# Kernel optimization log

Hardware: AMD Instinct MI355X
Metric: run time of the kernel (lower is better)

Reference implementation:

```python
import jax, jax.numpy as jnp
import numpy as np

NHEAD = 8
TOP_K = 2


def layernorm(x, g, b, eps=1e-5):
    m = x.mean(-1, keepdims=True)
    v = x.var(-1, keepdims=True)
    return (x - m) * jax.lax.rsqrt(v + eps) * g + b


def causal_conv(x, w, b, dil):
    # x: [N, C, L], w: [O, I, K] (torch layout), left-pad for causality
    pad = (w.shape[-1] - 1) * dil
    y = jax.lax.conv_general_dilated(x, w, (1,), [(pad, 0)], rhs_dilation=(dil,),
                                     dimension_numbers=('NCH', 'OIH', 'NCH'))
    return y + b[None, :, None]


def sinusoidal_pe(L, d):
    pos = jnp.arange(L, dtype=jnp.float32)[:, None]
    div = jnp.exp(jnp.arange(0, d, 2, dtype=jnp.float32) * (-np.log(10000.0) / d))
    pe = jnp.zeros((L, d), jnp.float32)
    pe = pe.at[:, 0::2].set(jnp.sin(pos * div))
    pe = pe.at[:, 1::2].set(jnp.cos(pos * div))
    return pe


def _forward(x, sensor_mask, enc_proj_w, enc_proj_b, tcn_w1, tcn_b1, tcn_w2, tcn_b2,
             enc_norm_g, enc_norm_b, pool_proj_w, pool_proj_b, pos_inter,
             t_wq, t_bq, t_wk, t_bk, t_wv, t_bv, t_wo, t_bo,
             t_ln1_g, t_ln1_b, t_ln2_g, t_ln2_b,
             t_ff1_w, t_ff1_b, t_ff2_w, t_ff2_b, t_out_g, t_out_b,
             exp_w1, exp_b1, exp_w2, exp_b2,
             gate_f_w, gate_f_b, gate_fail_w, gate_fail_b, gate_rca_w, gate_rca_b,
             pred_w, pred_b, fail_w, fail_b, rca_w, rca_b):
    B, L, M = x.shape
    P = enc_proj_w.shape[1]
    D = pool_proj_w.shape[1]
    O = exp_w2.shape[-1]
    # mask sensors, grab last value per sensor (globally standardized)
    xm = jnp.transpose(x, (0, 2, 1)) * sensor_mask[:, :, None]        # [B, M, L]
    last_val = xm[:, :, -1]                                           # [B, M]
    seqs = xm.reshape(B * M, L, 1)
    # per-sensor TCN encoder
    h = seqs @ enc_proj_w + enc_proj_b                                # [BM, L, P]
    h = h + sinusoidal_pe(L, P)[None]
    h = jnp.transpose(h, (0, 2, 1))                                   # [BM, P, L]
    for i in range(tcn_w1.shape[0]):
        dil = 2 ** i
        out = jax.nn.relu(causal_conv(h, tcn_w1[i], tcn_b1[i], dil))
        out = jax.nn.relu(causal_conv(out, tcn_w2[i], tcn_b2[i], dil))
        h = jax.nn.relu(out + h)                                      # channels equal -> identity residual
    h = layernorm(jnp.transpose(h, (0, 2, 1)), enc_norm_g, enc_norm_b)  # [BM, L, T]
    feats = h.reshape(B, M, L, -1) * sensor_mask[:, :, None, None]
    pooled = feats.mean(axis=2)                                       # [B, M, T]
    t = pooled @ pool_proj_w + pool_proj_b                            # [B, M, D]
    # inter-sensor transformer (pre-LN), key padding mask where sensor_mask==0
    t = t + pos_inter[:, :M, :]
    bias = jnp.where(sensor_mask == 0, -1e9, 0.0)[:, None, None, :]   # [B,1,1,M]
    dh = D // NHEAD
    for l in range(t_wq.shape[0]):
        y = layernorm(t, t_ln1_g[l], t_ln1_b[l])
        q = (y @ t_wq[l] + t_bq[l]).reshape(B, M, NHEAD, dh)
        k = (y @ t_wk[l] + t_bk[l]).reshape(B, M, NHEAD, dh)
        v = (y @ t_wv[l] + t_bv[l]).reshape(B, M, NHEAD, dh)
        s = jnp.einsum('bqhd,bkhd->bhqk', q, k) / jnp.sqrt(jnp.float32(dh)) + bias
        a = jax.nn.softmax(s, axis=-1)
        o = jnp.einsum('bhqk,bkhd->bqhd', a, v).reshape(B, M, D) @ t_wo[l] + t_bo[l]
        t = t + o
        y2 = layernorm(t, t_ln2_g[l], t_ln2_b[l])
        t = t + jax.nn.relu(y2 @ t_ff1_w[l] + t_ff1_b[l]) @ t_ff2_w[l] + t_ff2_b[l]
    ctx = layernorm(t, t_out_g, t_out_b) * sensor_mask[:, :, None]    # [B, M, D]
    # global context: masked mean + masked max over valid sensors
    cnt = jnp.maximum(sensor_mask.sum(1, keepdims=True), 1.0)
    mean_ctx = ctx.sum(1) / cnt                                       # [B, D]
    max_ctx = jnp.where(sensor_mask[:, :, None] > 0, ctx, -1e9).max(1)
    g = jnp.concatenate([mean_ctx, max_ctx], -1)                      # [B, 2D]

    def moe(x_exp, gate_in, gw, gb):
        logits = gate_in @ gw + gb                                    # [N, E]
        vals, idx = jax.lax.top_k(logits, TOP_K)
        w = jax.nn.softmax(vals, -1)
        hh = jax.nn.relu(jnp.einsum('nd,edh->neh', x_exp, exp_w1) + exp_b1)
        allo = jnp.einsum('neh,eho->neo', hh, exp_w2) + exp_b2        # [N, E, O]
        sel = jnp.take_along_axis(allo, idx[..., None], axis=1)
        return (sel * w[..., None]).sum(1)                            # [N, O]

    y_f = moe(g, g, gate_f_w, gate_f_b)                               # [B, O]
    y_fail = moe(g, g, gate_fail_w, gate_fail_b)
    tok = ctx.reshape(B * M, D)
    exp_in_rca = jnp.concatenate(
        [tok, jnp.broadcast_to(mean_ctx[:, None, :], (B, M, D)).reshape(B * M, D)], -1)
    y_rca = moe(exp_in_rca, tok, gate_rca_w, gate_rca_b).reshape(B, M, O)
    # heads
    pred_in = jnp.concatenate([pooled, ctx, jnp.broadcast_to(y_f[:, None, :], (B, M, O))], -1)
    pred = pred_in @ pred_w + pred_b + last_val[..., None]            # [B, M, PH]
    fail_out = y_fail @ fail_w + fail_b                               # [B, FH]
    rca_in = jnp.concatenate([pooled, ctx, y_rca], -1)
    rca_out = (rca_in @ rca_w + rca_b)[..., 0]                        # [B, M]
    return jnp.concatenate([pred.reshape(B, -1), fail_out, rca_out], axis=1)


def setup_inputs() -> dict:
    key = jax.random.key(0)
    ks = iter(jax.random.split(key, 64))
    nrm = lambda shape, s=0.05: jax.random.normal(next(ks), shape, jnp.float32) * s
    B, L, M = 16, 512, 32
    P, T, D, E, EH, O = 64, 64, 128, 16, 512, 128
    NL, LEV, K = 2, 4, 3
    return dict(
        x=jax.random.normal(next(ks), (B, L, M), jnp.float32),
        sensor_mask=jax.random.randint(next(ks), (B, M), 0, 2).astype(jnp.float32),
        enc_proj_w=nrm((1, P)), enc_proj_b=jnp.zeros((P,)),
        tcn_w1=nrm((LEV, P, P, K)), tcn_b1=jnp.zeros((LEV, P)),
        tcn_w2=nrm((LEV, P, P, K)), tcn_b2=jnp.zeros((LEV, P)),
        enc_norm_g=jnp.ones((T,)), enc_norm_b=jnp.zeros((T,)),
        pool_proj_w=nrm((T, D)), pool_proj_b=jnp.zeros((D,)),
        pos_inter=nrm((1, M, D), 0.02),
        t_wq=nrm((NL, D, D)), t_bq=jnp.zeros((NL, D)),
        t_wk=nrm((NL, D, D)), t_bk=jnp.zeros((NL, D)),
        t_wv=nrm((NL, D, D)), t_bv=jnp.zeros((NL, D)),
        t_wo=nrm((NL, D, D)), t_bo=jnp.zeros((NL, D)),
        t_ln1_g=jnp.ones((NL, D)), t_ln1_b=jnp.zeros((NL, D)),
        t_ln2_g=jnp.ones((NL, D)), t_ln2_b=jnp.zeros((NL, D)),
        t_ff1_w=nrm((NL, D, 2 * D)), t_ff1_b=jnp.zeros((NL, 2 * D)),
        t_ff2_w=nrm((NL, 2 * D, D)), t_ff2_b=jnp.zeros((NL, D)),
        t_out_g=jnp.ones((D,)), t_out_b=jnp.zeros((D,)),
        exp_w1=nrm((E, 2 * D, EH)), exp_b1=jnp.zeros((E, EH)),
        exp_w2=nrm((E, EH, O)), exp_b2=jnp.zeros((E, O)),
        gate_f_w=nrm((2 * D, E)), gate_f_b=jnp.zeros((E,)),
        gate_fail_w=nrm((2 * D, E)), gate_fail_b=jnp.zeros((E,)),
        gate_rca_w=nrm((D, E)), gate_rca_b=jnp.zeros((E,)),
        pred_w=nrm((T + D + O, 3)), pred_b=jnp.zeros((3,)),
        fail_w=nrm((O, 3)), fail_b=jnp.zeros((3,)),
        rca_w=nrm((T + D + O, 1)), rca_b=jnp.zeros((1,)),
    )


def reference(x, sensor_mask, enc_proj_w, enc_proj_b, tcn_w1, tcn_b1, tcn_w2, tcn_b2,
              enc_norm_g, enc_norm_b, pool_proj_w, pool_proj_b, pos_inter,
              t_wq, t_bq, t_wk, t_bk, t_wv, t_bv, t_wo, t_bo,
              t_ln1_g, t_ln1_b, t_ln2_g, t_ln2_b,
              t_ff1_w, t_ff1_b, t_ff2_w, t_ff2_b, t_out_g, t_out_b,
              exp_w1, exp_b1, exp_w2, exp_b2,
              gate_f_w, gate_f_b, gate_fail_w, gate_fail_b, gate_rca_w, gate_rca_b,
              pred_w, pred_b, fail_w, fail_b, rca_w, rca_b):
    return _forward(x, sensor_mask, enc_proj_w, enc_proj_b, tcn_w1, tcn_b1, tcn_w2, tcn_b2,
                    enc_norm_g, enc_norm_b, pool_proj_w, pool_proj_b, pos_inter,
                    t_wq, t_bq, t_wk, t_bk, t_wv, t_bv, t_wo, t_bo,
                    t_ln1_g, t_ln1_b, t_ln2_g, t_ln2_b,
                    t_ff1_w, t_ff1_b, t_ff2_w, t_ff2_b, t_out_g, t_out_b,
                    exp_w1, exp_b1, exp_w2, exp_b2,
                    gate_f_w, gate_f_b, gate_fail_w, gate_fail_b, gate_rca_w, gate_rca_b,
                    pred_w, pred_b, fail_w, fail_b, rca_w, rca_b)
```

## Files before the change

kernel.cpp:

```cpp
#include <hip/hip_runtime.h>
#include <hip/hip_bf16.h>

#define B_   16
#define L_   512
#define M_   32
#define P_   64
#define D_   128
#define NH_  8
#define NL_  2
#define E_   16
#define EH_  512
#define O_   128

#define PADF  16
#define ROWSF 528
#define LDW   64

typedef short  bf16x8 __attribute__((ext_vector_type(8)));
typedef float  f32x4  __attribute__((ext_vector_type(4)));
typedef unsigned short us4 __attribute__((ext_vector_type(4)));
typedef unsigned short us8 __attribute__((ext_vector_type(8)));

__device__ __forceinline__ float bf2f(unsigned short h) {
  unsigned u = ((unsigned)h) << 16; float f; __builtin_memcpy(&f, &u, 4); return f;
}
__device__ __forceinline__ unsigned short f2bf(float f) {
  unsigned u; __builtin_memcpy(&u, &f, 4);
  u += 0x7fffu + ((u >> 16) & 1);
  return (unsigned short)(u >> 16);
}
__device__ __forceinline__ int swz(int row, int col_us) {
  return row * LDW + (col_us ^ ((row & 7) << 3));
}

#define XFW_PPW   0
#define XFW_QKVO  8192
#define XFW_F1    139264
#define XFW_F2    204800

__global__ __launch_bounds__(256) void prep_kernel(
    const float* __restrict__ ppw,
    const float* __restrict__ twq, const float* __restrict__ twk,
    const float* __restrict__ twv, const float* __restrict__ two,
    const float* __restrict__ f1w, const float* __restrict__ f2w,
    const float* __restrict__ ew1, const float* __restrict__ ew2,
    const float* __restrict__ tw1, const float* __restrict__ tw2,
    unsigned short* __restrict__ xfw, unsigned short* __restrict__ w1t,
    unsigned short* __restrict__ w2t, unsigned short* __restrict__ wpack,
    float* __restrict__ peT) {
  const int b = blockIdx.x;
  const int tid = threadIdx.x;
  if (b < 834) {
    __shared__ float tl[64][65];
    const float* src; unsigned short* dst; int R, C, tr, tc;
    if (b < 2) {
      src = ppw; dst = xfw + XFW_PPW; R = 64; C = 128; tr = 0; tc = b;
    } else if (b < 34) {
      int t = b - 2; int lg = t >> 2; int l = lg >> 2, gem = lg & 3;
      int tt = t & 3; tr = tt >> 1; tc = tt & 1;
      const float* s4 = (gem == 0) ? twq : (gem == 1) ? twk : (gem == 2) ? twv : two;
      src = s4 + l * 16384; dst = xfw + XFW_QKVO + l * 65536 + gem * 16384; R = 128; C = 128;
    } else if (b < 50) {
      int t = b - 34; int l = t >> 3; int tt = t & 7; tr = tt >> 2; tc = tt & 3;
      src = f1w + l * 32768; dst = xfw + XFW_F1 + l * 32768; R = 128; C = 256;
    } else if (b < 66) {
      int t = b - 50; int l = t >> 3; int tt = t & 7; tr = tt >> 1; tc = tt & 1;
      src = f2w + l * 32768; dst = xfw + XFW_F2 + l * 32768; R = 256; C = 128;
    } else if (b < 578) {
      int t = b - 66; int e = t >> 5; int tt = t & 31; tr = tt >> 3; tc = tt & 7;
      src = ew1 + e * 131072; dst = w1t + e * 131072; R = 256; C = 512;
    } else {
      int t = b - 578; int e = t >> 4; int tt = t & 15; tr = tt >> 1; tc = tt & 1;
      src = ew2 + e * 65536; dst = w2t + e * 65536; R = 512; C = 128;
    }
    for (int i = tid; i < 4096; i += 256) {
      int r = i >> 6, c = i & 63;
      tl[r][c] = src[(tr * 64 + r) * C + tc * 64 + c];
    }
    __syncthreads();
    for (int i = tid; i < 4096; i += 256) {
      int c = i >> 6, r = i & 63;
      dst[(tc * 64 + c) * R + tr * 64 + r] = f2bf(tl[r][c]);
    }
  } else if (b < 840) {
    int base = (b - 834) * 16384;
    for (int q = tid; q < 16384; q += 256) {
      int i = base + q;
      int c = i & 63, o = (i >> 6) & 63, tlc = i >> 12;
      int t = tlc % 3, lc = tlc / 3, lvl = lc >> 1;
      const float* src = (lc & 1) ? tw2 : tw1;
      wpack[i] = f2bf(src[lvl * 12288 + o * 192 + c * 3 + t]);
    }
  } else {
    int base = (b - 840) * 16384;
    for (int q = tid; q < 16384; q += 256) {
      int j = base + q; int ll = j >> 6, c = j & 63;
      float dv = expf(-0.14391157f * (float)(c & ~1));
      float ang = (float)ll * dv;
      peT[j] = (c & 1) ? cosf(ang) : sinf(ang);
    }
  }
}

template <int DIL, bool RES>
__device__ __forceinline__ void conv_gw(const unsigned short* __restrict__ IN,
                                        unsigned short* __restrict__ OUT,
                                        const unsigned short* __restrict__ wp,
                                        const float* __restrict__ bias) {
  const int tid  = threadIdx.x;
  const int wid  = tid >> 6;
  const int lane = tid & 63;
  const int fr   = lane & 15;
  const int g    = lane >> 4;
  const int ot0  = (wid & 1) * 2;
  const int ng   = wid >> 1;

  bf16x8 Af[2][6];
#pragma unroll
  for (int oo = 0; oo < 2; ++oo)
#pragma unroll
    for (int t = 0; t < 3; ++t)
#pragma unroll
      for (int kh = 0; kh < 2; ++kh)
        Af[oo][t * 2 + kh] =
            *(const bf16x8*)(wp + (t * 64 + (ot0 + oo) * 16 + fr) * 64 + kh * 32 + g * 8);
  float bv[2][4];
#pragma unroll
  for (int oo = 0; oo < 2; ++oo)
#pragma unroll
    for (int j = 0; j < 4; ++j) bv[oo][j] = bias[(ot0 + oo) * 16 + g * 4 + j];

#pragma unroll
  for (int k = 0; k < 4; ++k) {
    const int rb = PADF + (ng + k * 8) * 16 + fr;
    bf16x8 Bf[6];
#pragma unroll
    for (int t = 0; t < 3; ++t) {
      int r = rb + (t - 2) * DIL;
#pragma unroll
      for (int kh = 0; kh < 2; ++kh)
        Bf[t * 2 + kh] = *(const bf16x8*)(IN + swz(r, kh * 32 + g * 8));
    }
    f32x4 acc[2];
#pragma unroll
    for (int oo = 0; oo < 2; ++oo) {
      f32x4 a; a[0] = bv[oo][0]; a[1] = bv[oo][1]; a[2] = bv[oo][2]; a[3] = bv[oo][3];
      acc[oo] = a;
    }
#pragma unroll
    for (int f = 0; f < 6; ++f)
#pragma unroll
      for (int oo = 0; oo < 2; ++oo)
        acc[oo] = __builtin_amdgcn_mfma_f32_16x16x32_bf16(Af[oo][f], Bf[f], acc[oo], 0, 0, 0);

#pragma unroll
    for (int oo = 0; oo < 2; ++oo) {
      unsigned short* op = OUT + swz(rb, (ot0 + oo) * 16 + g * 4);
      us4 old;
      if (RES) old = *(const us4*)op;
      us4 st;
#pragma unroll
      for (int j = 0; j < 4; ++j) {
        float v = fmaxf(acc[oo][j], 0.f);
        if (RES) v = fmaxf(v + bf2f(old[j]), 0.f);
        st[j] = f2bf(v);
      }
      *(us4*)op = st;
    }
  }
}

__global__ __launch_bounds__(1024) void tcn_kernel(
    const float* __restrict__ x, const float* __restrict__ mask,
    const float* __restrict__ pw, const float* __restrict__ pb,
    const unsigned short* __restrict__ wpack,
    const float* __restrict__ b1, const float* __restrict__ b2,
    const float* __restrict__ peT,
    const float* __restrict__ lng, const float* __restrict__ lnb,
    float* __restrict__ psum) {
  extern __shared__ unsigned short smu[];
  unsigned short* A  = smu;
  unsigned short* Bq = A + ROWSF * LDW;
  float* pwpb = (float*)(Bq + ROWSF * LDW);
  float* mst  = pwpb + 128;
  float* pp   = mst + 1024;

  const int seq = blockIdx.x;
  const int b = seq >> 5;
  const int m = seq & 31;
  if (mask[b * M_ + m] == 0.0f) return;
  const int tid = threadIdx.x;

  if (tid < 64)        pwpb[tid] = pw[tid];
  else if (tid < 128)  pwpb[tid] = pb[tid - 64];
  __syncthreads();

  if (tid < ROWSF) {
    int r = tid;
    if (r >= PADF) {
      int l = r - PADF;
      float xv = x[(b * L_ + l) * M_ + m];
      const float4* pe4 = (const float4*)(peT + l * 64);
#pragma unroll
      for (int c0 = 0; c0 < 64; c0 += 8) {
        float4 pa = pe4[c0 / 4], pc = pe4[c0 / 4 + 1];
        float pe[8] = {pa.x, pa.y, pa.z, pa.w, pc.x, pc.y, pc.z, pc.w};
        us8 st;
#pragma unroll
        for (int j = 0; j < 8; ++j) {
          int c = c0 + j;
          st[j] = f2bf(fmaf(xv, pwpb[c], pwpb[64 + c]) + pe[j]);
        }
        *(us8*)(A + swz(r, c0)) = st;
      }
    } else {
      us8 z = {0, 0, 0, 0, 0, 0, 0, 0};
#pragma unroll
      for (int c0 = 0; c0 < 64; c0 += 8) {
        *(us8*)(A + swz(r, c0)) = z;
        *(us8*)(Bq + swz(r, c0)) = z;
      }
    }
  }
  __syncthreads();

  conv_gw<1, false>(A, Bq, wpack + 0 * 12288, b1 + 0);   __syncthreads();
  conv_gw<1, true >(Bq, A, wpack + 1 * 12288, b2 + 0);   __syncthreads();
  conv_gw<2, false>(A, Bq, wpack + 2 * 12288, b1 + 64);  __syncthreads();
  conv_gw<2, true >(Bq, A, wpack + 3 * 12288, b2 + 64);  __syncthreads();
  conv_gw<4, false>(A, Bq, wpack + 4 * 12288, b1 + 128); __syncthreads();
  conv_gw<4, true >(Bq, A, wpack + 5 * 12288, b2 + 128); __syncthreads();
  conv_gw<8, false>(A, Bq, wpack + 6 * 12288, b1 + 192); __syncthreads();
  conv_gw<8, true >(Bq, A, wpack + 7 * 12288, b2 + 192); __syncthreads();

  if (tid < 512) {
    int r = PADF + tid;
    float s = 0.f, ss = 0.f;
#pragma unroll
    for (int c0 = 0; c0 < 64; c0 += 8) {
      bf16x8 vv = *(const bf16x8*)(A + swz(r, c0));
#pragma unroll
      for (int j = 0; j < 8; ++j) { float v = bf2f((unsigned short)vv[j]); s += v; ss += v * v; }
    }
    float mu = s * 0.015625f;
    float var = fmaxf(ss * 0.015625f - mu * mu, 0.0f);
    mst[tid] = mu;
    mst[512 + tid] = rsqrtf(var + 1e-5f);
  }
  __syncthreads();
  {
    int p = tid & 63, q = tid >> 6;
    float accp = 0.f;
    int r0 = PADF + q * 32;
    for (int r = r0; r < r0 + 32; ++r)
      accp += (bf2f(A[swz(r, p)]) - mst[r - PADF]) * mst[512 + r - PADF];
    pp[tid] = accp;
  }
  __syncthreads();
  if (tid < 64) {
    float acc = 0.f;
#pragma unroll
    for (int q = 0; q < 16; ++q) acc += pp[q * 64 + tid];
    psum[seq * 64 + tid] = lng[tid] * acc + 512.0f * lnb[tid];
  }
}

__global__ __launch_bounds__(1024) void xf_kernel(
    const float* __restrict__ psum, const float* __restrict__ mask,
    const unsigned short* __restrict__ xfw,
    const float* __restrict__ ppb, const float* __restrict__ pos,
    const float* __restrict__ bq, const float* __restrict__ bk,
    const float* __restrict__ bv, const float* __restrict__ bo,
    const float* __restrict__ l1g, const float* __restrict__ l1b,
    const float* __restrict__ l2g, const float* __restrict__ l2b,
    const float* __restrict__ f1b, const float* __restrict__ f2b,
    const float* __restrict__ og_, const float* __restrict__ ob_,
    const float* __restrict__ gfw, const float* __restrict__ gfb,
    const float* __restrict__ glw, const float* __restrict__ glb,
    const float* __restrict__ grw, const float* __restrict__ grb,
    float* __restrict__ pooledws, float* __restrict__ ctxws,
    float* __restrict__ gwt, int* __restrict__ ecnt, int* __restrict__ elist,
    unsigned short* __restrict__ xbf) {
  extern __shared__ float sm[];
  float* T    = sm;
  float* QKV  = T + 4224;
  float* S    = QKV + 12672;
  float* gv   = S + 8448;
  float* mkv  = gv + 512;
  unsigned short* Ybf = (unsigned short*)(mkv + 64);
  unsigned short* Yb2 = Ybf + 32 * 136;
  unsigned short* FFH = Yb2 + 32 * 136;
  const int b = blockIdx.x;
  const int tid = threadIdx.x;
  const int wid = tid >> 6;
  const int lane = tid & 63;
  const int fr = lane & 15;
  const int g = lane >> 4;
  const int row32 = tid >> 5;
  const int ln32  = tid & 31;

  if (tid < 32) mkv[tid] = mask[b * 32 + tid];
  for (int idx = tid; idx < 2048; idx += 1024) {
    int mm = idx >> 6, p = idx & 63;
    float v = psum[(b * 32 + mm) * 64 + p] * mask[b * 32 + mm] * (1.0f / 512.0f);
    pooledws[(b * 32 + mm) * 64 + p] = v;
    Ybf[mm * 136 + p] = f2bf(v);
  }
  __syncthreads();

  {
    int mt = wid >> 3, nt = wid & 7;
    bf16x8 Af[2];
#pragma unroll
    for (int kf = 0; kf < 2; ++kf)
      Af[kf] = *(const bf16x8*)(Ybf + (mt * 16 + fr) * 136 + kf * 32 + g * 8);
    const unsigned short* bp = xfw + XFW_PPW + (nt * 16 + fr) * 64;
    f32x4 acc = {0.f, 0.f, 0.f, 0.f};
#pragma unroll
    for (int kf = 0; kf < 2; ++kf)
      acc = __builtin_amdgcn_mfma_f32_16x16x32_bf16(Af[kf], *(const bf16x8*)(bp + kf * 32 + g * 8), acc, 0, 0, 0);
    int n = nt * 16 + fr;
    float bb = ppb[n];
#pragma unroll
    for (int j = 0; j < 4; ++j) {
      int m = mt * 16 + g * 4 + j;
      T[m * 132 + n] = acc[j] + bb + pos[m * 128 + n];
    }
  }
  __syncthreads();

#define LN_BF(GAMMA, BETA)                                                     \
  {                                                                            \
    int mm = row32, j0 = ln32 * 4;                                             \
    float4 v4 = *(const float4*)(T + mm * 132 + j0);                           \
    float s = v4.x + v4.y + v4.z + v4.w;                                       \
    float ss = v4.x * v4.x + v4.y * v4.y + v4.z * v4.z + v4.w * v4.w;          \
    _Pragma("unroll") for (int mk = 16; mk >= 1; mk >>= 1) {                   \
      s += __shfl_xor(s, mk); ss += __shfl_xor(ss, mk);                        \
    }                                                                          \
    float mu = s * 0.0078125f;                                                 \
    float rstd = rsqrtf(fmaxf(ss * 0.0078125f - mu * mu, 0.f) + 1e-5f);        \
    us4 st;                                                                    \
    float vv[4] = {v4.x, v4.y, v4.z, v4.w};                                    \
    _Pragma("unroll") for (int j = 0; j < 4; ++j)                              \
      st[j] = f2bf((vv[j] - mu) * rstd * (GAMMA)[j0 + j] + (BETA)[j0 + j]);    \
    *(us4*)(Ybf + mm * 136 + j0) = st;                                         \
  }                                                                            \
  __syncthreads();

  for (int l = 0; l < NL_; ++l) {
    LN_BF(l1g + l * 128, l1b + l * 128)
#pragma unroll
    for (int i = 0; i < 3; ++i) {
      int tt = wid * 3 + i;
      int gem = tt >> 4, r = tt & 15, mt = r >> 3, nt = r & 7;
      const unsigned short* wT = xfw + XFW_QKVO + l * 65536 + gem * 16384;
      const float* bias = (gem == 0) ? bq : (gem == 1) ? bk : bv;
      bf16x8 Afr[4];
#pragma unroll
      for (int kf = 0; kf < 4; ++kf)
        Afr[kf] = *(const bf16x8*)(Ybf + (mt * 16 + fr) * 136 + kf * 32 + g * 8);
      const unsigned short* bp = wT + (nt * 16 + fr) * 128;
      f32x4 acc = {0.f, 0.f, 0.f, 0.f};
#pragma unroll
      for (int kf = 0; kf < 4; ++kf)
        acc = __builtin_amdgcn_mfma_f32_16x16x32_bf16(Afr[kf], *(const bf16x8*)(bp + kf * 32 + g * 8), acc, 0, 0, 0);
      int n = nt * 16 + fr;
      float bb = bias[l * 128 + n];
#pragma unroll
      for (int j = 0; j < 4; ++j)
        QKV[(mt * 16 + g * 4 + j) * 396 + gem * 132 + n] = acc[j] + bb;
    }
    __syncthreads();

    {
      int n = ln32;
      float mbias = (mkv[n] == 0.0f) ? -1e9f : 0.f;
#pragma unroll
      for (int t = 0; t < 8; ++t) {
        int task = row32 * 8 + t;
        int h = task >> 5, mm = task & 31;
        const float* qp = QKV + mm * 396 + h * 16;
        const float* kp = QKV + n * 396 + 132 + h * 16;
        float a = 0;
#pragma unroll
        for (int d = 0; d < 16; ++d) a = fmaf(qp[d], kp[d], a);
        a = a * 0.25f + mbias;
        float mx = a;
#pragma unroll
        for (int mk = 16; mk >= 1; mk >>= 1) mx = fmaxf(mx, __shfl_xor(mx, mk));
        float e = __expf(a - mx);
        float sum = e;
#pragma unroll
        for (int mk = 16; mk >= 1; mk >>= 1) sum += __shfl_xor(sum, mk);
        S[h * 1056 + mm * 33 + n] = e / sum;
      }
    }
    __syncthreads();

    {
      int mm = row32, j0 = ln32 * 4, h = j0 >> 4;
      const float* sp = S + h * 1056 + mm * 33;
      f32x4 a = {0.f, 0.f, 0.f, 0.f};
#pragma unroll 8
      for (int n = 0; n < 32; ++n) {
        float p = sp[n];
        float4 v4 = *(const float4*)(QKV + n * 396 + 264 + j0);
        a[0] = fmaf(p, v4.x, a[0]); a[1] = fmaf(p, v4.y, a[1]);
        a[2] = fmaf(p, v4.z, a[2]); a[3] = fmaf(p, v4.w, a[3]);
      }
      us4 st;
#pragma unroll
      for (int j = 0; j < 4; ++j) st[j] = f2bf(a[j]);
      *(us4*)(Yb2 + mm * 136 + j0) = st;
    }
    __syncthreads();

    {
      int mt = wid >> 3, nt = wid & 7;
      bf16x8 Aw[4];
#pragma unroll
      for (int kf = 0; kf < 4; ++kf)
        Aw[kf] = *(const bf16x8*)(Yb2 + (mt * 16 + fr) * 136 + kf * 32 + g * 8);
      const unsigned short* bp = xfw + XFW_QKVO + l * 65536 + 3 * 16384 + (nt * 16 + fr) * 128;
      f32x4 acc = {0.f, 0.f, 0.f, 0.f};
#pragma unroll
      for (int kf = 0; kf < 4; ++kf)
        acc = __builtin_amdgcn_mfma_f32_16x16x32_bf16(Aw[kf], *(const bf16x8*)(bp + kf * 32 + g * 8), acc, 0, 0, 0);
      int n = nt * 16 + fr;
      float bb = bo[l * 128 + n];
#pragma unroll
      for (int j = 0; j < 4; ++j)
        T[(mt * 16 + g * 4 + j) * 132 + n] += acc[j] + bb;
    }
    __syncthreads();

    LN_BF(l2g + l * 128, l2b + l * 128)
#pragma unroll
    for (int i = 0; i < 2; ++i) {
      int tt = wid * 2 + i;
      int mt = tt >> 4, nt = tt & 15;
      bf16x8 Aff[4];
#pragma unroll
      for (int kf = 0; kf < 4; ++kf)
        Aff[kf] = *(const bf16x8*)(Ybf + (mt * 16 + fr) * 136 + kf * 32 + g * 8);
      const unsigned short* bp = xfw + XFW_F1 + l * 32768 + (nt * 16 + fr) * 128;
      f32x4 acc = {0.f, 0.f, 0.f, 0.f};
#pragma unroll
      for (int kf = 0; kf < 4; ++kf)
        acc = __builtin_amdgcn_mfma_f32_16x16x32_bf16(Aff[kf], *(const bf16x8*)(bp + kf * 32 + g * 8), acc, 0, 0, 0);
      int n = nt * 16 + fr;
      float bb = f1b[l * 256 + n];
#pragma unroll
      for (int j = 0; j < 4; ++j)
        FFH[(mt * 16 + g * 4 + j) * 264 + n] = f2bf(fmaxf(acc[j] + bb, 0.f));
    }
    __syncthreads();
    {
      int mt = wid >> 3, nt = wid & 7;
      bf16x8 Af2[8];
#pragma unroll
      for (int kf = 0; kf < 8; ++kf)
        Af2[kf] = *(const bf16x8*)(FFH + (mt * 16 + fr) * 264 + kf * 32 + g * 8);
      const unsigned short* bp = xfw + XFW_F2 + l * 32768 + (nt * 16 + fr) * 256;
      f32x4 acc = {0.f, 0.f, 0.f, 0.f};
#pragma unroll
      for (int kf = 0; kf < 8; ++kf)
        acc = __builtin_amdgcn_mfma_f32_16x16x32_bf16(Af2[kf], *(const bf16x8*)(bp + kf * 32 + g * 8), acc, 0, 0, 0);
      int n = nt * 16 + fr;
      float bb = f2b[l * 128 + n];
#pragma unroll
      for (int j = 0; j < 4; ++j)
        T[(mt * 16 + g * 4 + j) * 132 + n] += acc[j] + bb;
    }
    __syncthreads();
  }
#undef LN_BF

  {
    int mm = row32, j0 = ln32 * 4;
    float4 v4 = *(const float4*)(T + mm * 132 + j0);
    float s = v4.x + v4.y + v4.z + v4.w;
    float ss = v4.x * v4.x + v4.y * v4.y + v4.z * v4.z + v4.w * v4.w;
#pragma unroll
    for (int mk = 16; mk >= 1; mk >>= 1) { s += __shfl_xor(s, mk); ss += __shfl_xor(ss, mk); }
    float mu = s * 0.0078125f;
    float rstd = rsqrtf(fmaxf(ss * 0.0078125f - mu * mu, 0.f) + 1e-5f);
    float mk_ = mkv[mm];
    float vv[4] = {v4.x, v4.y, v4.z, v4.w};
#pragma unroll
    for (int j = 0; j < 4; ++j) {
      float c = ((vv[j] - mu) * rstd * og_[j0 + j] + ob_[j0 + j]) * mk_;
      S[mm * 132 + j0 + j] = c;
      ctxws[(b * 32 + mm) * 128 + j0 + j] = c;
    }
  }
  __syncthreads();
  if (tid < 128) {
    float cnt = 0;
    for (int mm = 0; mm < 32; ++mm) cnt += mkv[mm];
    cnt = fmaxf(cnt, 1.0f);
    float s = 0, mx = -1e9f;
    for (int mm = 0; mm < 32; ++mm) {
      float v = S[mm * 132 + tid];
      s += v;
      if (mkv[mm] > 0.0f) mx = fmaxf(mx, v);
    }
    gv[tid] = s / cnt;
    gv[128 + tid] = mx;
  }
  __syncthreads();

  float* lg = QKV;
  if (tid < 544) {
    int lr = tid >> 4, e = tid & 15;
    float a;
    if (lr == 0) {
      a = gfb[e];
      for (int d = 0; d < 256; ++d) a = fmaf(gv[d], gfw[d * 16 + e], a);
    } else if (lr == 1) {
      a = glb[e];
      for (int d = 0; d < 256; ++d) a = fmaf(gv[d], glw[d * 16 + e], a);
    } else {
      int mm = lr - 2;
      a = grb[e];
      for (int d = 0; d < 128; ++d) a = fmaf(S[mm * 132 + d], grw[d * 16 + e], a);
    }
    lg[lr * 16 + e] = a;
  }
  __syncthreads();
  if (tid < 34) {
    const float* lgr = lg + tid * 16;
    int i0 = 0; float v0 = lgr[0];
    for (int e = 1; e < 16; ++e) if (lgr[e] > v0) { v0 = lgr[e]; i0 = e; }
    int i1 = (i0 == 0) ? 1 : 0; float v1 = lgr[i1];
    for (int e = 0; e < 16; ++e) if (e != i0 && lgr[e] > v1) { v1 = lgr[e]; i1 = e; }
    float e1 = __expf(v1 - v0);
    float w0 = 1.0f / (1.0f + e1);
    int gr = (tid == 0) ? b : (tid == 1) ? (16 + b) : (32 + b * 32 + (tid - 2));
    gwt[2 * gr] = w0;  gwt[2 * gr + 1] = 1.0f - w0;
    int p0 = atomicAdd(&ecnt[i0], 1); elist[i0 * 544 + p0] = 2 * gr;
    int p1 = atomicAdd(&ecnt[i1], 1); elist[i1 * 544 + p1] = 2 * gr + 1;
  }
  for (int j = tid; j < 34 * 256; j += 1024) {
    int lr = j >> 8, d = j & 255;
    float v;
    if (lr < 2) v = gv[d];
    else        v = (d < 128) ? S[(lr - 2) * 132 + d] : gv[d - 128];
    int gr = (lr == 0) ? b : (lr == 1) ? (16 + b) : (32 + b * 32 + (lr - 2));
    xbf[gr * 256 + d] = f2bf(v);
  }
}

__global__ __launch_bounds__(512) void moe_kernel(
    const unsigned short* __restrict__ xbf, const float* __restrict__ gwt,
    const int* __restrict__ elist, const int* __restrict__ ecnt,
    const unsigned short* __restrict__ w1t, const float* __restrict__ eb1,
    const unsigned short* __restrict__ w2t, const float* __restrict__ eb2,
    float* __restrict__ yall) {
  __shared__ unsigned short Xb[16 * 264];
  __shared__ unsigned short Hb[16 * 520];
  __shared__ float wl[16];
  __shared__ int rowl[16];
  const int e = blockIdx.x >> 3;
  const int slot = blockIdx.x & 7;
  const int n = ecnt[e];
  const int ntiles = (n + 15) >> 4;
  const int tid = threadIdx.x;
  const int wid = tid >> 6;
  const int lane = tid & 63;
  const int fr = lane & 15;
  const int g = lane >> 4;

  for (int t = slot; t < ntiles; t += 8) {
    if (tid < 16) {
      int idx = t * 16 + tid;
      int id = (idx < n) ? elist[e * 544 + idx] : -1;
      rowl[tid] = (id >= 0) ? (id >> 1) : -1;
      wl[tid] = (id >= 0) ? gwt[id] : 0.f;
    }
    __syncthreads();
    for (int i = tid; i < 512; i += 512) {
      int r = i >> 5, c8 = (i & 31) * 8;
      int row = rowl[r];
      bf16x8 v = {0, 0, 0, 0, 0, 0, 0, 0};
      if (row >= 0) v = *(const bf16x8*)(xbf + row * 256 + c8);
      *(bf16x8*)(Xb + r * 264 + c8) = v;
    }
    __syncthreads();
    bf16x8 Af[8];
#pragma unroll
    for (int kf = 0; kf < 8; ++kf)
      Af[kf] = *(const bf16x8*)(Xb + fr * 264 + kf * 32 + g * 8);
#pragma unroll
    for (int ntl = 0; ntl < 4; ++ntl) {
      int nt = wid * 4 + ntl;
      const unsigned short* bp = w1t + (e * 512 + nt * 16 + fr) * 256;
      f32x4 acc = {0.f, 0.f, 0.f, 0.f};
#pragma unroll
      for (int kf = 0; kf < 8; ++kf)
        acc = __builtin_amdgcn_mfma_f32_16x16x32_bf16(Af[kf], *(const bf16x8*)(bp + kf * 32 + g * 8), acc, 0, 0, 0);
      int h = nt * 16 + fr;
      float b1v = eb1[e * 512 + h];
#pragma unroll
      for (int j = 0; j < 4; ++j)
        Hb[(g * 4 + j) * 520 + h] = f2bf(fmaxf(acc[j] + b1v, 0.f));
    }
    __syncthreads();
    {
      const unsigned short* bp = w2t + (e * 128 + wid * 16 + fr) * 512;
      f32x4 acc = {0.f, 0.f, 0.f, 0.f};
#pragma unroll
      for (int kf = 0; kf < 16; ++kf) {
        bf16x8 Ah = *(const bf16x8*)(Hb + fr * 520 + kf * 32 + g * 8);
        acc = __builtin_amdgcn_mfma_f32_16x16x32_bf16(Ah, *(const bf16x8*)(bp + kf * 32 + g * 8), acc, 0, 0, 0);
      }
      int o = wid * 16 + fr;
      float b2v = eb2[e * 128 + o];
#pragma unroll
      for (int j = 0; j < 4; ++j) {
        int r = g * 4 + j;
        int row = rowl[r];
        if (row >= 0) atomicAdd(&yall[row * 128 + o], wl[r] * (acc[j] + b2v));
      }
    }
    __syncthreads();
  }
}

__global__ __launch_bounds__(192) void heads_kernel(
    const float* __restrict__ x, const float* __restrict__ mask,
    const float* __restrict__ pooledws, const float* __restrict__ ctxws,
    const float* __restrict__ yf, const float* __restrict__ yfail, const float* __restrict__ yrca,
    const float* __restrict__ pw, const float* __restrict__ pb,
    const float* __restrict__ fw, const float* __restrict__ fb,
    const float* __restrict__ rw, const float* __restrict__ rb,
    float* __restrict__ out) {
  __shared__ float yfb[128];
  int b = blockIdx.x, t = threadIdx.x;
  if (t < 128) yfb[t] = yf[b * 128 + t];
  __syncthreads();
  if (t < 96) {
    int mm = t / 3, o = t - mm * 3;
    int s = b * 32 + mm;
    float a = pb[o];
    const float* pl = pooledws + s * 64;
    for (int i = 0; i < 64; ++i) a = fmaf(pl[i], pw[i * 3 + o], a);
    const float* cx = ctxws + s * 128;
    for (int i = 0; i < 128; ++i) a = fmaf(cx[i], pw[(64 + i) * 3 + o], a);
    for (int i = 0; i < 128; ++i) a = fmaf(yfb[i], pw[(192 + i) * 3 + o], a);
    a += x[(b * 512 + 511) * 32 + mm] * mask[b * 32 + mm];
    out[b * 131 + t] = a;
  } else if (t < 99) {
    int o = t - 96;
    float a = fb[o];
    const float* yl = yfail + b * 128;
    for (int i = 0; i < 128; ++i) a = fmaf(yl[i], fw[i * 3 + o], a);
    out[b * 131 + 96 + o] = a;
  } else if (t < 131) {
    int mm = t - 99;
    int s = b * 32 + mm;
    float a = rb[0];
    const float* pl = pooledws + s * 64;
    for (int i = 0; i < 64; ++i) a = fmaf(pl[i], rw[i], a);
    const float* cx = ctxws + s * 128;
    for (int i = 0; i < 128; ++i) a = fmaf(cx[i], rw[64 + i], a);
    const float* yr = yrca + s * 128;
    for (int i = 0; i < 128; ++i) a = fmaf(yr[i], rw[192 + i], a);
    out[b * 131 + 99 + mm] = a;
  }
}

extern "C" void kernel_launch(void* const* d_in, const int* in_sizes, int n_in,
                              void* d_out, int out_size, void* d_ws, size_t ws_size,
                              hipStream_t stream) {
  (void)in_sizes; (void)n_in; (void)out_size; (void)ws_size;
  const float* x    = (const float*)d_in[0];
  const float* msk  = (const float*)d_in[1];
  const float* epw  = (const float*)d_in[2];
  const float* epb  = (const float*)d_in[3];
  const float* tw1  = (const float*)d_in[4];
  const float* tb1  = (const float*)d_in[5];
  const float* tw2  = (const float*)d_in[6];
  const float* tb2  = (const float*)d_in[7];
  const float* eng  = (const float*)d_in[8];
  const float* enb  = (const float*)d_in[9];
  const float* ppw  = (const float*)d_in[10];
  const float* ppb  = (const float*)d_in[11];
  const float* pos  = (const float*)d_in[12];
  const float* twq  = (const float*)d_in[13];
  const float* tbq  = (const float*)d_in[14];
  const float* twk  = (const float*)d_in[15];
  const float* tbk  = (const float*)d_in[16];
  const float* twv  = (const float*)d_in[17];
  const float* tbv  = (const float*)d_in[18];
  const float* two  = (const float*)d_in[19];
  const float* tbo  = (const float*)d_in[20];
  const float* l1g  = (const float*)d_in[21];
  const float* l1b  = (const float*)d_in[22];
  const float* l2g  = (const float*)d_in[23];
  const float* l2b  = (const float*)d_in[24];
  const float* f1w  = (const float*)d_in[25];
  const float* f1b  = (const float*)d_in[26];
  const float* f2w  = (const float*)d_in[27];
  const float* f2b  = (const float*)d_in[28];
  const float* tog  = (const float*)d_in[29];
  const float* tob  = (const float*)d_in[30];
  const float* ew1  = (const float*)d_in[31];
  const float* eb1  = (const float*)d_in[32];
  const float* ew2  = (const float*)d_in[33];
  const float* eb2  = (const float*)d_in[34];
  const float* gfw  = (const float*)d_in[35];
  const float* gfb  = (const float*)d_in[36];
  const float* glw  = (const float*)d_in[37];
  const float* glb  = (const float*)d_in[38];
  const float* grw  = (const float*)d_in[39];
  const float* grb  = (const float*)d_in[40];
  const float* prw  = (const float*)d_in[41];
  const float* prb  = (const float*)d_in[42];
  const float* fw   = (const float*)d_in[43];
  const float* fb   = (const float*)d_in[44];
  const float* rw   = (const float*)d_in[45];
  const float* rb   = (const float*)d_in[46];

  float* ws      = (float*)d_ws;
  float* psum    = ws;
  float* pooledw = psum + 32768;
  float* ctxw    = pooledw + 32768;
  float* yall    = ctxw + 65536;
  float* gwt     = yall + 69632;
  int*   ecnt    = (int*)(gwt + 1088);
  int*   elist   = ecnt + 16;
  float* peT     = (float*)(elist + 8704);
  unsigned short* wpack = (unsigned short*)(peT + 32768);
  unsigned short* xfw   = wpack + 98304;
  unsigned short* w1t   = xfw + 270336;
  unsigned short* w2t   = w1t + 2097152;
  unsigned short* xbf   = w2t + 1048576;

  const int tcn_lds = 2 * ROWSF * LDW * 2 + (128 + 1024 + 1024) * 4;
  const int xf_lds  = (4224 + 12672 + 8448 + 512 + 64) * 4 + (2 * 4352 + 8448) * 2;
  hipFuncSetAttribute((const void*)tcn_kernel, hipFuncAttributeMaxDynamicSharedMemorySize, tcn_lds);
  hipFuncSetAttribute((const void*)xf_kernel,  hipFuncAttributeMaxDynamicSharedMemorySize, xf_lds);

  hipMemsetAsync(yall, 0, 69632 * sizeof(float), stream);
  hipMemsetAsync(ecnt, 0, 16 * sizeof(int), stream);

  prep_kernel<<<842, 256, 0, stream>>>(ppw, twq, twk, twv, two, f1w, f2w, ew1, ew2,
                                       tw1, tw2, xfw, w1t, w2t, wpack, peT);
  tcn_kernel<<<512, 1024, tcn_lds, stream>>>(x, msk, epw, epb, wpack, tb1, tb2, peT,
                                             eng, enb, psum);
  xf_kernel<<<16, 1024, xf_lds, stream>>>(psum, msk, xfw, ppb, pos,
                                          tbq, tbk, tbv, tbo,
                                          l1g, l1b, l2g, l2b, f1b, f2b,
                                          tog, tob,
                                          gfw, gfb, glw, glb, grw, grb,
                                          pooledw, ctxw, gwt, ecnt, elist, xbf);
  moe_kernel<<<128, 512, 0, stream>>>(xbf, gwt, elist, ecnt, w1t, eb1, w2t, eb2, yall);
  heads_kernel<<<16, 192, 0, stream>>>(x, msk, pooledw, ctxw,
                                       yall, yall + 2048, yall + 4096,
                                       prw, prb, fw, fb, rw, rb, (float*)d_out);
}
```

Before: 290.2 us.

## Stage TCN conv weights in LDS with register prefetch; fold memsets into prep

The TCN kernel now stages each level's packed conv weights into a swizzled LDS buffer. The next level's weights are prefetched from global memory into registers while the current convolution runs, replacing per-wave global loads of the A fragments. The LN scratch now aliases the weight buffer, which shrinks LDS, and waves_per_eu is set for occupancy. The two hipMemsetAsync calls are folded into extra prep_kernel blocks, and the workspace layout is shifted, at the cost of extra register pressure and syncs per phase.

```diff
diff --git a/kernel.cpp b/kernel.cpp
--- a/kernel.cpp
+++ b/kernel.cpp
@@ -47,7 +47,7 @@
     const float* __restrict__ tw1, const float* __restrict__ tw2,
     unsigned short* __restrict__ xfw, unsigned short* __restrict__ w1t,
     unsigned short* __restrict__ w2t, unsigned short* __restrict__ wpack,
-    float* __restrict__ peT) {
+    float* __restrict__ peT, float* __restrict__ yall, int* __restrict__ ecnt) {
   const int b = blockIdx.x;
   const int tid = threadIdx.x;
   if (b < 834) {
@@ -91,7 +91,7 @@
       const float* src = (lc & 1) ? tw2 : tw1;
       wpack[i] = f2bf(src[lvl * 12288 + o * 192 + c * 3 + t]);
     }
-  } else {
+  } else if (b < 842) {
     int base = (b - 840) * 16384;
     for (int q = tid; q < 16384; q += 256) {
       int j = base + q; int ll = j >> 6, c = j & 63;
@@ -99,14 +99,23 @@
       float ang = (float)ll * dv;
       peT[j] = (c & 1) ? cosf(ang) : sinf(ang);
     }
+  } else {
+    int j = b - 842;
+    if (j < 68) {
+      for (int q = tid; q < 1024; q += 256) yall[j * 1024 + q] = 0.f;
+    } else {
+      if (tid < 16) ecnt[tid] = 0;
+    }
   }
 }
 
 template <int DIL, bool RES>
-__device__ __forceinline__ void conv_gw(const unsigned short* __restrict__ IN,
-                                        unsigned short* __restrict__ OUT,
-                                        const unsigned short* __restrict__ wp,
-                                        const float* __restrict__ bias) {
+__device__ __forceinline__ void conv_phase(const unsigned short* __restrict__ IN,
+                                           unsigned short* __restrict__ OUT,
+                                           unsigned short* __restrict__ Wb,
+                                           const float* __restrict__ bias,
+                                           float4* wreg, bool do_store,
+                                           const unsigned short* __restrict__ wload) {
   const int tid  = threadIdx.x;
   const int wid  = tid >> 6;
   const int lane = tid & 63;
@@ -121,14 +130,28 @@
 #pragma unroll
     for (int t = 0; t < 3; ++t)
 #pragma unroll
-      for (int kh = 0; kh < 2; ++kh)
-        Af[oo][t * 2 + kh] =
-            *(const bf16x8*)(wp + (t * 64 + (ot0 + oo) * 16 + fr) * 64 + kh * 32 + g * 8);
+      for (int kh = 0; kh < 2; ++kh) {
+        int wr = t * 64 + (ot0 + oo) * 16 + fr;
+        Af[oo][t * 2 + kh] = *(const bf16x8*)(Wb + swz(wr, kh * 32 + g * 8));
+      }
   float bv[2][4];
 #pragma unroll
   for (int oo = 0; oo < 2; ++oo)
 #pragma unroll
     for (int j = 0; j < 4; ++j) bv[oo][j] = bias[(ot0 + oo) * 16 + g * 4 + j];
+
+  __syncthreads();
+
+  if (do_store) {
+    *(float4*)(Wb + swz(tid >> 3, (tid & 7) * 8)) = wreg[0];
+    if (tid < 512)
+      *(float4*)(Wb + swz((tid >> 3) + 128, (tid & 7) * 8)) = wreg[1];
+  }
+  if (wload) {
+    wreg[0] = *(const float4*)(wload + (tid >> 3) * 64 + (tid & 7) * 8);
+    if (tid < 512)
+      wreg[1] = *(const float4*)(wload + ((tid >> 3) + 128) * 64 + (tid & 7) * 8);
+  }
 
 #pragma unroll
   for (int k = 0; k < 4; ++k) {
@@ -168,9 +191,12 @@
       *(us4*)op = st;
     }
   }
-}
-
-__global__ __launch_bounds__(1024) void tcn_kernel(
+  __syncthreads();
+}
+
+__global__ __attribute__((amdgpu_flat_work_group_size(1024, 1024),
+                          amdgpu_waves_per_eu(4, 4)))
+void tcn_kernel(
     const float* __restrict__ x, const float* __restrict__ mask,
     const float* __restrict__ pw, const float* __restrict__ pb,
     const unsigned short* __restrict__ wpack,
@@ -181,8 +207,9 @@
   extern __shared__ unsigned short smu[];
   unsigned short* A  = smu;
   unsigned short* Bq = A + ROWSF * LDW;
-  float* pwpb = (float*)(Bq + ROWSF * LDW);
-  float* mst  = pwpb + 128;
+  unsigned short* Wb = Bq + ROWSF * LDW;
+  float* pwpb = (float*)(Wb + 192 * LDW);
+  float* mst  = (float*)Wb;
   float* pp   = mst + 1024;
 
   const int seq = blockIdx.x;
@@ -191,8 +218,12 @@
   if (mask[b * M_ + m] == 0.0f) return;
   const int tid = threadIdx.x;
 
-  if (tid < 64)        pwpb[tid] = pw[tid];
-  else if (tid < 128)  pwpb[tid] = pb[tid - 64];
+  float4 wreg[2];
+  wreg[0] = *(const float4*)(wpack + (tid >> 3) * 64 + (tid & 7) * 8);
+  if (tid < 512)
+    wreg[1] = *(const float4*)(wpack + ((tid >> 3) + 128) * 64 + (tid & 7) * 8);
+  if (tid < 64)       pwpb[tid] = pw[tid];
+  else if (tid < 128) pwpb[tid] = pb[tid - 64];
   __syncthreads();
 
   if (tid < ROWSF) {
@@ -224,14 +255,24 @@
   }
   __syncthreads();
 
-  conv_gw<1, false>(A, Bq, wpack + 0 * 12288, b1 + 0);   __syncthreads();
-  conv_gw<1, true >(Bq, A, wpack + 1 * 12288, b2 + 0);   __syncthreads();
-  conv_gw<2, false>(A, Bq, wpack + 2 * 12288, b1 + 64);  __syncthreads();
-  conv_gw<2, true >(Bq, A, wpack + 3 * 12288, b2 + 64);  __syncthreads();
-  conv_gw<4, false>(A, Bq, wpack + 4 * 12288, b1 + 128); __syncthreads();
-  conv_gw<4, true >(Bq, A, wpack + 5 * 12288, b2 + 128); __syncthreads();
-  conv_gw<8, false>(A, Bq, wpack + 6 * 12288, b1 + 192); __syncthreads();
-  conv_gw<8, true >(Bq, A, wpack + 7 * 12288, b2 + 192); __syncthreads();
+  {
+    *(float4*)(Wb + swz(tid >> 3, (tid & 7) * 8)) = wreg[0];
+    if (tid < 512)
+      *(float4*)(Wb + swz((tid >> 3) + 128, (tid & 7) * 8)) = wreg[1];
+    wreg[0] = *(const float4*)(wpack + 12288 + (tid >> 3) * 64 + (tid & 7) * 8);
+    if (tid < 512)
+      wreg[1] = *(const float4*)(wpack + 12288 + ((tid >> 3) + 128) * 64 + (tid & 7) * 8);
+  }
+  __syncthreads();
+
+  conv_phase<1, false>(A, Bq, Wb, b1 + 0,   wreg, true, wpack + 2 * 12288);
+  conv_phase<1, true >(Bq, A, Wb, b2 + 0,   wreg, true, wpack + 3 * 12288);
+  conv_phase<2, false>(A, Bq, Wb, b1 + 64,  wreg, true, wpack + 4 * 12288);
+  conv_phase<2, true >(Bq, A, Wb, b2 + 64,  wreg, true, wpack + 5 * 12288);
+  conv_phase<4, false>(A, Bq, Wb, b1 + 128, wreg, true, wpack + 6 * 12288);
+  conv_phase<4, true >(Bq, A, Wb, b2 + 128, wreg, true, wpack + 7 * 12288);
+  conv_phase<8, false>(A, Bq, Wb, b1 + 192, wreg, true, (const unsigned short*)nullptr);
+  conv_phase<8, true >(Bq, A, Wb, b2 + 192, wreg, false, (const unsigned short*)nullptr);
 
   if (tid < 512) {
     int r = PADF + tid;
@@ -265,7 +306,7 @@
   }
 }
 
-__global__ __launch_bounds__(1024) void xf_kernel(
+__global__ __launch_bounds__(1024, 1) void xf_kernel(
     const float* __restrict__ psum, const float* __restrict__ mask,
     const unsigned short* __restrict__ xfw,
     const float* __restrict__ ppb, const float* __restrict__ pos,
@@ -725,7 +766,7 @@
 
   float* ws      = (float*)d_ws;
   float* psum    = ws;
-  float* pooledw = psum + 32768;
+  float* pooledw = psum + 65536;
   float* ctxw    = pooledw + 32768;
   float* yall    = ctxw + 65536;
   float* gwt     = yall + 69632;
@@ -738,16 +779,13 @@
   unsigned short* w2t   = w1t + 2097152;
   unsigned short* xbf   = w2t + 1048576;
 
-  const int tcn_lds = 2 * ROWSF * LDW * 2 + (128 + 1024 + 1024) * 4;
+  const int tcn_lds = 2 * ROWSF * LDW * 2 + 192 * LDW * 2 + 128 * 4;
   const int xf_lds  = (4224 + 12672 + 8448 + 512 + 64) * 4 + (2 * 4352 + 8448) * 2;
   hipFuncSetAttribute((const void*)tcn_kernel, hipFuncAttributeMaxDynamicSharedMemorySize, tcn_lds);
   hipFuncSetAttribute((const void*)xf_kernel,  hipFuncAttributeMaxDynamicSharedMemorySize, xf_lds);
 
-  hipMemsetAsync(yall, 0, 69632 * sizeof(float), stream);
-  hipMemsetAsync(ecnt, 0, 16 * sizeof(int), stream);
-
-  prep_kernel<<<842, 256, 0, stream>>>(ppw, twq, twk, twv, two, f1w, f2w, ew1, ew2,
-                                       tw1, tw2, xfw, w1t, w2t, wpack, peT);
+  prep_kernel<<<911, 256, 0, stream>>>(ppw, twq, twk, twv, two, f1w, f2w, ew1, ew2,
+                                       tw1, tw2, xfw, w1t, w2t, wpack, peT, yall, ecnt);
   tcn_kernel<<<512, 1024, tcn_lds, stream>>>(x, msk, epw, epb, wpack, tb1, tb2, peT,
                                              eng, enb, psum);
   xf_kernel<<<16, 1024, xf_lds, stream>>>(psum, msk, xfw, ppb, pos,
```

New measurement: 265.8 us. -8.4%, faster.
